# Kernel tuning notes

Hardware: AMD Instinct MI355X
Metric: run time of the kernel (lower is better)

## Reference

```python
import jax, jax.numpy as jnp
import numpy as np

NUM_EXPERTS = 8
TOP_K = 2


def setup_inputs() -> dict:
    key = jax.random.key(0)
    k1, k2, k3, k4, k5 = jax.random.split(key, 5)
    H, F, E = 1024, 4096, NUM_EXPERTS
    s = 0.02
    return {
        "hidden_states": jax.random.normal(k1, (2, 2048, H), jnp.float32),
        "w_router": jax.random.normal(k2, (E, H), jnp.float32) * s,
        "w1": jax.random.normal(k3, (E, F, H), jnp.float32) * s,
        "w2": jax.random.normal(k4, (E, H, F), jnp.float32) * s,
        "w3": jax.random.normal(k5, (E, F, H), jnp.float32) * s,
    }


def reference(hidden_states, w_router, w1, w2, w3):
    B, S, H = hidden_states.shape
    x = hidden_states.reshape(-1, H)  # [T, H]
    T = x.shape[0]
    # router (nn.Linear, no bias): logits = x @ W^T
    router_logits = x @ w_router.T  # [T, E]
    probs = jax.nn.softmax(router_logits.astype(jnp.float32), axis=-1)
    top_w, top_e = jax.lax.top_k(probs, TOP_K)  # [T, K]
    top_w = top_w / jnp.sum(top_w, axis=-1, keepdims=True)
    top_w = top_w.astype(x.dtype)
    # dense per-token gate matrix [T, E]; zero where expert not selected
    gates = jnp.zeros((T, NUM_EXPERTS), x.dtype).at[
        jnp.arange(T)[:, None], top_e
    ].add(top_w)
    out = jnp.zeros_like(x)
    for e in range(NUM_EXPERTS):  # fixed small expert loop
        h = jax.nn.silu(x @ w1[e].T) * (x @ w3[e].T)  # [T, F]
        out = out + gates[:, e:e + 1] * (h @ w2[e].T)
    return out.reshape(B, S, H), router_logits
```

## Files before the change

kernel.cpp:

```cpp
#include <hip/hip_runtime.h>
#include <hip/hip_bf16.h>
#include <stdint.h>

#define T_TOK 4096
#define H_DIM 1024
#define F_DIM 4096
#define NE 8
#define MG_BLKS 40

typedef float    f32x4  __attribute__((ext_vector_type(4)));
typedef __bf16   bf16x8 __attribute__((ext_vector_type(8)));
typedef uint16_t u16x8  __attribute__((ext_vector_type(8)));

#define AS1 __attribute__((address_space(1)))
#define AS3 __attribute__((address_space(3)))

__device__ __forceinline__ uint16_t f2bf(float f) {
  return __builtin_bit_cast(uint16_t, __float2bfloat16(f));
}

__device__ __forceinline__ void gld16(const void* g, void* l) {
  __builtin_amdgcn_global_load_lds((const AS1 void*)g, (AS3 void*)l, 16, 0, 0);
}

__device__ __forceinline__ bf16x8 ldsB_frag(const float* tile, int row, int kg) {
  const int p0 = (2 * kg) ^ (row & 15);
  const int p1 = (2 * kg + 1) ^ (row & 15);
  const f32x4 v0 = *(const f32x4*)&tile[row * 64 + p0 * 4];
  const f32x4 v1 = *(const f32x4*)&tile[row * 64 + p1 * 4];
  u16x8 ub;
#pragma unroll
  for (int j = 0; j < 4; ++j) { ub[j] = f2bf(v0[j]); ub[j + 4] = f2bf(v1[j]); }
  return __builtin_bit_cast(bf16x8, ub);
}

__device__ __forceinline__ void calc_base(const int* cnt, int* base9) {
  int b = 0;
#pragma unroll
  for (int e = 0; e < NE; ++e) { base9[e] = b; b += (cnt[e] + 255) & ~255; }
  base9[NE] = b;
}

__global__ __launch_bounds__(256) void router_k(
    const float* __restrict__ x, const float* __restrict__ wr,
    float* __restrict__ logits, uint16_t* __restrict__ xb,
    int* __restrict__ pairTok, float* __restrict__ pairGate,
    int* __restrict__ cnt)
{
  const int lane = threadIdx.x & 63;
  const int wid  = threadIdx.x >> 6;
  const int t    = blockIdx.x * 4 + wid;

  const float* xp = x + (size_t)t * H_DIM + lane * 16;
  f32x4 xv[4];
#pragma unroll
  for (int i = 0; i < 4; ++i) xv[i] = *(const f32x4*)(xp + 4 * i);

  u16x8 o0, o1;
#pragma unroll
  for (int j = 0; j < 4; ++j) {
    o0[j] = f2bf(xv[0][j]); o0[j + 4] = f2bf(xv[1][j]);
    o1[j] = f2bf(xv[2][j]); o1[j + 4] = f2bf(xv[3][j]);
  }
  uint16_t* xbp = xb + (size_t)t * H_DIM + lane * 16;
  *(u16x8*)xbp       = o0;
  *(u16x8*)(xbp + 8) = o1;

  float s[NE];
#pragma unroll
  for (int e = 0; e < NE; ++e) {
    const float* wp = wr + e * H_DIM + lane * 16;
    float acc = 0.f;
#pragma unroll
    for (int i = 0; i < 4; ++i) {
      f32x4 wv = *(const f32x4*)(wp + 4 * i);
#pragma unroll
      for (int j = 0; j < 4; ++j) acc += xv[i][j] * wv[j];
    }
#pragma unroll
    for (int off = 32; off > 0; off >>= 1) acc += __shfl_xor(acc, off, 64);
    s[e] = acc;
  }

  if (lane == 0) {
#pragma unroll
    for (int e = 0; e < NE; ++e) logits[t * NE + e] = s[e];
    int e1 = 0;
#pragma unroll
    for (int e = 1; e < NE; ++e) if (s[e] > s[e1]) e1 = e;
    int e2 = (e1 == 0) ? 1 : 0;
#pragma unroll
    for (int e = 0; e < NE; ++e)
      if (e != e1 && e != e2 && s[e] > s[e2]) e2 = e;
    const float d  = s[e2] - s[e1];
    const float g1 = 1.f / (1.f + __expf(d));
    const float g2 = 1.f - g1;
    int i1 = atomicAdd(cnt + e1, 1);
    pairTok[e1 * T_TOK + i1] = t;  pairGate[e1 * T_TOK + i1] = g1;
    int i2 = atomicAdd(cnt + e2, 1);
    pairTok[e2 * T_TOK + i2] = t;  pairGate[e2 * T_TOK + i2] = g2;
  }
}

__global__ __launch_bounds__(256, 2) void ffn1_k(
    const uint16_t* __restrict__ xb, const float* __restrict__ w1,
    const float* __restrict__ w3, uint16_t* __restrict__ hbuf,
    const int* __restrict__ pairTok, const float* __restrict__ pairGate,
    const int* __restrict__ cnt)
{
  int base[NE + 1];
  calc_base(cnt, base);
  const int mg0 = blockIdx.y * 256;
  if (mg0 >= base[NE]) return;
  int e = 0;
#pragma unroll
  for (int k = 1; k < NE; ++k) if (mg0 >= base[k]) e = k;
  const int m0   = mg0 - base[e];
  const int cnte = cnt[e];
  const int n0   = blockIdx.x * 64;
  const int tid  = threadIdx.x;
  const int lane = tid & 63;
  const int wid  = tid >> 6;
  const int wm   = (wid >> 1) * 128;
  const int wn   = (wid & 1) * 32;

  __shared__ __align__(16) uint16_t lsA [256 * 64];
  __shared__ __align__(16) float    lsB1[ 64 * 64];
  __shared__ __align__(16) float    lsB3[ 64 * 64];

  const float* w1e = w1 + (size_t)e * F_DIM * H_DIM;
  const float* w3e = w3 + (size_t)e * F_DIM * H_DIM;

  const uint16_t* asrc[8];
#pragma unroll
  for (int q = 0; q < 8; ++q) {
    const int c = q * 256 + tid;
    const int row = c >> 3, pos = c & 7;
    const int kc  = pos ^ (row & 7);
    int ar = m0 + row; if (ar >= cnte) ar = cnte - 1;
    const int tok = pairTok[e * T_TOK + ar];
    asrc[q] = xb + (size_t)tok * H_DIM + kc * 8;
  }
  const float* b1src[4];
  const float* b3src[4];
#pragma unroll
  for (int q = 0; q < 4; ++q) {
    const int c = q * 256 + tid;
    const int row = c >> 4, pos = c & 15;
    const int kc  = pos ^ (row & 15);
    b1src[q] = w1e + (size_t)(n0 + row) * H_DIM + kc * 4;
    b3src[q] = w3e + (size_t)(n0 + row) * H_DIM + kc * 4;
  }

  const f32x4 fz = {0.f, 0.f, 0.f, 0.f};
  f32x4 acc1[8][2], acc3[8][2];
#pragma unroll
  for (int i = 0; i < 8; ++i)
#pragma unroll
    for (int j = 0; j < 2; ++j) { acc1[i][j] = fz; acc3[i][j] = fz; }

  for (int kt = 0; kt < H_DIM; kt += 64) {
    __syncthreads();
#pragma unroll
    for (int q = 0; q < 8; ++q)
      gld16(asrc[q] + kt, &lsA[(q * 256 + tid) * 8]);
#pragma unroll
    for (int q = 0; q < 4; ++q) {
      gld16(b1src[q] + kt, &lsB1[(q * 256 + tid) * 4]);
      gld16(b3src[q] + kt, &lsB3[(q * 256 + tid) * 4]);
    }
    __syncthreads();
#pragma unroll
    for (int ks = 0; ks < 2; ++ks) {
      const int kg = ks * 4 + (lane >> 4);
      bf16x8 af[8], b1f[2], b3f[2];
#pragma unroll
      for (int i = 0; i < 8; ++i) {
        const int ar = wm + i * 16 + (lane & 15);
        af[i] = *(const bf16x8*)&lsA[ar * 64 + ((kg ^ (ar & 7)) * 8)];
      }
#pragma unroll
      for (int j = 0; j < 2; ++j) {
        const int br = wn + j * 16 + (lane & 15);
        b1f[j] = ldsB_frag(lsB1, br, kg);
        b3f[j] = ldsB_frag(lsB3, br, kg);
      }
#pragma unroll
      for (int i = 0; i < 8; ++i)
#pragma unroll
        for (int j = 0; j < 2; ++j) {
          acc1[i][j] = __builtin_amdgcn_mfma_f32_16x16x32_bf16(af[i], b1f[j], acc1[i][j], 0, 0, 0);
          acc3[i][j] = __builtin_amdgcn_mfma_f32_16x16x32_bf16(af[i], b3f[j], acc3[i][j], 0, 0, 0);
        }
    }
  }

  const int be = base[e];
#pragma unroll
  for (int i = 0; i < 8; ++i) {
#pragma unroll
    for (int rr = 0; rr < 4; ++rr) {
      const int lrow = m0 + wm + i * 16 + (lane >> 4) * 4 + rr;
      if (lrow < cnte) {
        const float g = pairGate[e * T_TOK + lrow];
        uint16_t* hp = hbuf + (size_t)(be + lrow) * F_DIM + n0 + wn + (lane & 15);
#pragma unroll
        for (int j = 0; j < 2; ++j) {
          const float a  = acc1[i][j][rr];
          const float hv = g * (a / (1.f + __expf(-a))) * acc3[i][j][rr];
          hp[j * 16] = f2bf(hv);
        }
      }
    }
  }
}

__global__ __launch_bounds__(256, 2) void ffn2_k(
    const uint16_t* __restrict__ hbuf, const float* __restrict__ w2,
    float* __restrict__ out, const int* __restrict__ pairTok,
    const int* __restrict__ cnt)
{
  int base[NE + 1];
  calc_base(cnt, base);
  const int mg0 = blockIdx.y * 256;
  if (mg0 >= base[NE]) return;
  int e = 0;
#pragma unroll
  for (int k = 1; k < NE; ++k) if (mg0 >= base[k]) e = k;
  const int m0   = mg0 - base[e];
  const int cnte = cnt[e];
  const int n0   = blockIdx.x * 128;
  const int k0   = blockIdx.z * (F_DIM / 2);
  const int tid  = threadIdx.x;
  const int lane = tid & 63;
  const int wid  = tid >> 6;
  const int wm   = (wid >> 1) * 128;
  const int wn   = (wid & 1) * 64;

  __shared__ __align__(16) uint16_t lsA[256 * 64];
  __shared__ __align__(16) float    lsB[128 * 64];

  const int be = base[e];
  const float* w2e = w2 + (size_t)e * H_DIM * F_DIM;

  const uint16_t* asrc[8];
#pragma unroll
  for (int q = 0; q < 8; ++q) {
    const int c = q * 256 + tid;
    const int row = c >> 3, pos = c & 7;
    const int kc  = pos ^ (row & 7);
    int rr = m0 + row; if (rr >= cnte) rr = cnte - 1;
    asrc[q] = hbuf + (size_t)(be + rr) * F_DIM + k0 + kc * 8;
  }
  const float* bsrc[8];
#pragma unroll
  for (int q = 0; q < 8; ++q) {
    const int c = q * 256 + tid;
    const int row = c >> 4, pos = c & 15;
    const int kc  = pos ^ (row & 15);
    bsrc[q] = w2e + (size_t)(n0 + row) * F_DIM + k0 + kc * 4;
  }

  const f32x4 fz = {0.f, 0.f, 0.f, 0.f};
  f32x4 acc[8][4];
#pragma unroll
  for (int i = 0; i < 8; ++i)
#pragma unroll
    for (int j = 0; j < 4; ++j) acc[i][j] = fz;

  for (int kt = 0; kt < F_DIM / 2; kt += 64) {
    __syncthreads();
#pragma unroll
    for (int q = 0; q < 8; ++q)
      gld16(asrc[q] + kt, &lsA[(q * 256 + tid) * 8]);
#pragma unroll
    for (int q = 0; q < 8; ++q)
      gld16(bsrc[q] + kt, &lsB[(q * 256 + tid) * 4]);
    __syncthreads();
#pragma unroll
    for (int ks = 0; ks < 2; ++ks) {
      const int kg = ks * 4 + (lane >> 4);
      bf16x8 af[8], bf[4];
#pragma unroll
      for (int i = 0; i < 8; ++i) {
        const int ar = wm + i * 16 + (lane & 15);
        af[i] = *(const bf16x8*)&lsA[ar * 64 + ((kg ^ (ar & 7)) * 8)];
      }
#pragma unroll
      for (int j = 0; j < 4; ++j) {
        const int br = wn + j * 16 + (lane & 15);
        bf[j] = ldsB_frag(lsB, br, kg);
      }
#pragma unroll
      for (int i = 0; i < 8; ++i)
#pragma unroll
        for (int j = 0; j < 4; ++j)
          acc[i][j] = __builtin_amdgcn_mfma_f32_16x16x32_bf16(af[i], bf[j], acc[i][j], 0, 0, 0);
    }
  }

#pragma unroll
  for (int i = 0; i < 8; ++i) {
#pragma unroll
    for (int rr = 0; rr < 4; ++rr) {
      const int lrow = m0 + wm + i * 16 + (lane >> 4) * 4 + rr;
      if (lrow < cnte) {
        const int t = pairTok[e * T_TOK + lrow];
        float* op = out + (size_t)t * H_DIM + n0 + wn + (lane & 15);
#pragma unroll
        for (int j = 0; j < 4; ++j)
          unsafeAtomicAdd(op + j * 16, acc[i][j][rr]);
      }
    }
  }
}

extern "C" void kernel_launch(void* const* d_in, const int* in_sizes, int n_in,
                              void* d_out, int out_size, void* d_ws, size_t ws_size,
                              hipStream_t stream)
{
  const float* x  = (const float*)d_in[0];
  const float* wr = (const float*)d_in[1];
  const float* w1 = (const float*)d_in[2];
  const float* w2 = (const float*)d_in[3];
  const float* w3 = (const float*)d_in[4];
  float* out    = (float*)d_out;
  float* logits = out + (size_t)T_TOK * H_DIM;

  uint8_t* ws = (uint8_t*)d_ws;
  const size_t PADROWS  = (size_t)MG_BLKS * 256;
  const size_t XB_OFF   = 0;
  const size_t HB_OFF   = XB_OFF + (size_t)T_TOK * H_DIM * 2;
  const size_t PT_OFF   = HB_OFF + PADROWS * F_DIM * 2;
  const size_t PG_OFF   = PT_OFF + (size_t)NE * T_TOK * 4;
  const size_t CNT_OFF  = PG_OFF + (size_t)NE * T_TOK * 4;
  const size_t NEED     = CNT_OFF + 64;
  if (ws_size < NEED) return;

  uint16_t* xb      = (uint16_t*)(ws + XB_OFF);
  uint16_t* hb      = (uint16_t*)(ws + HB_OFF);
  int*      pairTok = (int*)(ws + PT_OFF);
  float*    pairGate= (float*)(ws + PG_OFF);
  int*      cnt     = (int*)(ws + CNT_OFF);

  hipMemsetAsync(out, 0, (size_t)T_TOK * H_DIM * sizeof(float), stream);
  hipMemsetAsync(cnt, 0, 64, stream);
  router_k<<<T_TOK / 4, 256, 0, stream>>>(x, wr, logits, xb, pairTok, pairGate, cnt);
  ffn1_k<<<dim3(F_DIM / 64, MG_BLKS, 1), 256, 0, stream>>>(xb, w1, w3, hb, pairTok, pairGate, cnt);
  ffn2_k<<<dim3(H_DIM / 128, MG_BLKS, 2), 256, 0, stream>>>(hb, w2, out, pairTok, cnt);
}
```

Baseline: 507.7 us.

## Replace atomic scatter in down-projection with bf16 staging and combine kernel

The down-projection kernel now writes its split-K partial results as bf16 into a per-expert-slot staging buffer instead of atomically adding fp32 values into the output. A new combine kernel gathers each token's two expert slots and both K halves, using a token-to-slot map recorded by the router, and writes the final output directly. This removes the output memset and the scattered fp32 atomics. In exchange it adds an extra kernel launch, a staging buffer round trip, and bf16 rounding of the partial sums.

```diff
diff --git a/kernel.cpp b/kernel.cpp
--- a/kernel.cpp
+++ b/kernel.cpp
@@ -7,6 +7,7 @@
 #define F_DIM 4096
 #define NE 8
 #define MG_BLKS 40
+#define PADROWS (MG_BLKS * 256)
 
 typedef float    f32x4  __attribute__((ext_vector_type(4)));
 typedef __bf16   bf16x8 __attribute__((ext_vector_type(8)));
@@ -17,6 +18,10 @@
 
 __device__ __forceinline__ uint16_t f2bf(float f) {
   return __builtin_bit_cast(uint16_t, __float2bfloat16(f));
+}
+
+__device__ __forceinline__ float bf2f(uint16_t u) {
+  return __bfloat162float(__hip_bfloat16_raw{u});
 }
 
 __device__ __forceinline__ void gld16(const void* g, void* l) {
@@ -45,7 +50,7 @@
     const float* __restrict__ x, const float* __restrict__ wr,
     float* __restrict__ logits, uint16_t* __restrict__ xb,
     int* __restrict__ pairTok, float* __restrict__ pairGate,
-    int* __restrict__ cnt)
+    int* __restrict__ tokSlot, int* __restrict__ cnt)
 {
   const int lane = threadIdx.x & 63;
   const int wid  = threadIdx.x >> 6;
@@ -99,6 +104,8 @@
     pairTok[e1 * T_TOK + i1] = t;  pairGate[e1 * T_TOK + i1] = g1;
     int i2 = atomicAdd(cnt + e2, 1);
     pairTok[e2 * T_TOK + i2] = t;  pairGate[e2 * T_TOK + i2] = g2;
+    int4 sl; sl.x = e1; sl.y = i1; sl.z = e2; sl.w = i2;
+    ((int4*)tokSlot)[t] = sl;
   }
 }
 
@@ -217,8 +224,7 @@
 
 __global__ __launch_bounds__(256, 2) void ffn2_k(
     const uint16_t* __restrict__ hbuf, const float* __restrict__ w2,
-    float* __restrict__ out, const int* __restrict__ pairTok,
-    const int* __restrict__ cnt)
+    uint16_t* __restrict__ y, const int* __restrict__ cnt)
 {
   int base[NE + 1];
   calc_base(cnt, base);
@@ -242,6 +248,7 @@
 
   const int be = base[e];
   const float* w2e = w2 + (size_t)e * H_DIM * F_DIM;
+  uint16_t* ybuf = y + (size_t)blockIdx.z * PADROWS * H_DIM;
 
   const uint16_t* asrc[8];
 #pragma unroll
@@ -305,14 +312,40 @@
     for (int rr = 0; rr < 4; ++rr) {
       const int lrow = m0 + wm + i * 16 + (lane >> 4) * 4 + rr;
       if (lrow < cnte) {
-        const int t = pairTok[e * T_TOK + lrow];
-        float* op = out + (size_t)t * H_DIM + n0 + wn + (lane & 15);
+        uint16_t* yp = ybuf + (size_t)(be + lrow) * H_DIM + n0 + wn + (lane & 15);
 #pragma unroll
         for (int j = 0; j < 4; ++j)
-          unsafeAtomicAdd(op + j * 16, acc[i][j][rr]);
-      }
-    }
-  }
+          yp[j * 16] = f2bf(acc[i][j][rr]);
+      }
+    }
+  }
+}
+
+__global__ __launch_bounds__(256) void combine_k(
+    const uint16_t* __restrict__ y, const int* __restrict__ tokSlot,
+    const int* __restrict__ cnt, float* __restrict__ out)
+{
+  int base[NE + 1];
+  calc_base(cnt, base);
+  const int t = blockIdx.x * 2 + (threadIdx.x >> 7);
+  const int c = (threadIdx.x & 127) * 8;
+  const int4 s = ((const int4*)tokSlot)[t];
+  const size_t r1 = (size_t)(base[s.x] + s.y) * H_DIM + c;
+  const size_t r2 = (size_t)(base[s.z] + s.w) * H_DIM + c;
+  const size_t HSTRIDE = (size_t)PADROWS * H_DIM;
+  const u16x8 a0 = *(const u16x8*)(y + r1);
+  const u16x8 a1 = *(const u16x8*)(y + HSTRIDE + r1);
+  const u16x8 b0 = *(const u16x8*)(y + r2);
+  const u16x8 b1 = *(const u16x8*)(y + HSTRIDE + r2);
+  float* op = out + (size_t)t * H_DIM + c;
+  f32x4 o0, o1;
+#pragma unroll
+  for (int j = 0; j < 4; ++j) {
+    o0[j] = bf2f(a0[j])     + bf2f(a1[j])     + bf2f(b0[j])     + bf2f(b1[j]);
+    o1[j] = bf2f(a0[j + 4]) + bf2f(a1[j + 4]) + bf2f(b0[j + 4]) + bf2f(b1[j + 4]);
+  }
+  *(f32x4*)op       = o0;
+  *(f32x4*)(op + 4) = o1;
 }
 
 extern "C" void kernel_launch(void* const* d_in, const int* in_sizes, int n_in,
@@ -328,24 +361,27 @@
   float* logits = out + (size_t)T_TOK * H_DIM;
 
   uint8_t* ws = (uint8_t*)d_ws;
-  const size_t PADROWS  = (size_t)MG_BLKS * 256;
   const size_t XB_OFF   = 0;
   const size_t HB_OFF   = XB_OFF + (size_t)T_TOK * H_DIM * 2;
-  const size_t PT_OFF   = HB_OFF + PADROWS * F_DIM * 2;
+  const size_t Y_OFF    = HB_OFF + (size_t)PADROWS * F_DIM * 2;
+  const size_t PT_OFF   = Y_OFF + (size_t)2 * PADROWS * H_DIM * 2;
   const size_t PG_OFF   = PT_OFF + (size_t)NE * T_TOK * 4;
-  const size_t CNT_OFF  = PG_OFF + (size_t)NE * T_TOK * 4;
+  const size_t TS_OFF   = PG_OFF + (size_t)NE * T_TOK * 4;
+  const size_t CNT_OFF  = TS_OFF + (size_t)T_TOK * 16;
   const size_t NEED     = CNT_OFF + 64;
   if (ws_size < NEED) return;
 
   uint16_t* xb      = (uint16_t*)(ws + XB_OFF);
   uint16_t* hb      = (uint16_t*)(ws + HB_OFF);
+  uint16_t* yb      = (uint16_t*)(ws + Y_OFF);
   int*      pairTok = (int*)(ws + PT_OFF);
   float*    pairGate= (float*)(ws + PG_OFF);
+  int*      tokSlot = (int*)(ws + TS_OFF);
   int*      cnt     = (int*)(ws + CNT_OFF);
 
-  hipMemsetAsync(out, 0, (size_t)T_TOK * H_DIM * sizeof(float), stream);
   hipMemsetAsync(cnt, 0, 64, stream);
-  router_k<<<T_TOK / 4, 256, 0, stream>>>(x, wr, logits, xb, pairTok, pairGate, cnt);
+  router_k<<<T_TOK / 4, 256, 0, stream>>>(x, wr, logits, xb, pairTok, pairGate, tokSlot, cnt);
   ffn1_k<<<dim3(F_DIM / 64, MG_BLKS, 1), 256, 0, stream>>>(xb, w1, w3, hb, pairTok, pairGate, cnt);
-  ffn2_k<<<dim3(H_DIM / 128, MG_BLKS, 2), 256, 0, stream>>>(hb, w2, out, pairTok, cnt);
-}
+  ffn2_k<<<dim3(H_DIM / 128, MG_BLKS, 2), 256, 0, stream>>>(hb, w2, yb, cnt);
+  combine_k<<<T_TOK / 2, 256, 0, stream>>>(yb, tokSlot, cnt, out);
+}
```

Measured after the change: 472.1 us. -7.0%, faster.
